# Kernel tuning notes

Measured on AMD Instinct MI355X. Metric: run time of the kernel, lower is better.

## Reference

```python
import jax, jax.numpy as jnp
import numpy as np

NUM_HEADS = 12

def setup_inputs() -> dict:
    key = jax.random.key(0)
    ks = jax.random.split(key, 6)
    B, Nq, Nkv, C = 2, 2048, 2048, 768
    q_token = jax.random.normal(ks[0], (B, Nq, C), dtype=jnp.float32)
    kv_token = jax.random.normal(ks[1], (B, Nkv, C), dtype=jnp.float32)
    s = 1.0 / np.sqrt(C)
    Wq = jax.random.normal(ks[2], (C, C), dtype=jnp.float32) * s
    Wkv = jax.random.normal(ks[3], (C, 2 * C), dtype=jnp.float32) * s
    Wproj = jax.random.normal(ks[4], (C, C), dtype=jnp.float32) * s
    bproj = jnp.zeros((C,), dtype=jnp.float32)
    return {"q_token": q_token, "kv_token": kv_token, "Wq": Wq, "Wkv": Wkv, "Wproj": Wproj, "bproj": bproj}

def reference(q_token, kv_token, Wq, Wkv, Wproj, bproj):
    B, Nq, C = q_token.shape
    H = NUM_HEADS
    D = C // H
    scale = D ** -0.5
    # Q: [B, H, Nq, D]
    Q = (q_token @ Wq).reshape(B, Nq, H, D).transpose(0, 2, 1, 3)
    # KV: token layout is (2, H, D) on last dim -> [2, B, H, Nkv, D]
    Nkv = kv_token.shape[1]
    KV = (kv_token @ Wkv).reshape(B, Nkv, 2, H, D).transpose(2, 0, 3, 1, 4)
    K, V = KV[0], KV[1]
    attn = jnp.einsum('bhqd,bhkd->bhqk', Q, K) * scale
    attn = jax.nn.softmax(attn, axis=-1)
    # NOTE: original code multiplies by scale again here (faithful quirk)
    x = jnp.einsum('bhqk,bhkd->bhqd', attn, V) * scale
    x = x.transpose(0, 2, 1, 3).reshape(B, Nq, C)
    return x @ Wproj + bproj
```

## Files before the change

kernel.cpp:

```cpp
#include <hip/hip_runtime.h>

typedef __attribute__((ext_vector_type(8))) short short8;
typedef __attribute__((ext_vector_type(4))) float f32x4;
typedef __attribute__((ext_vector_type(16))) float f32x16;
typedef __attribute__((ext_vector_type(4))) unsigned u32x4;

__device__ __forceinline__ unsigned short f2bf(float f) {
  unsigned u = __builtin_bit_cast(unsigned, f);
  u += 0x7fffu + ((u >> 16) & 1u);
  return (unsigned short)(u >> 16);
}

__device__ __forceinline__ unsigned cvt_pk_bf16(float a, float b) {
  unsigned r;
  asm("v_cvt_pk_bf16_f32 %0, %1, %2" : "=v"(r) : "v"(a), "v"(b));
  return r;
}

__device__ __forceinline__ void gload_lds16(const unsigned short* g, unsigned short* l) {
  __builtin_amdgcn_global_load_lds((const __attribute__((address_space(1))) unsigned int*)g,
                                   (__attribute__((address_space(3))) unsigned int*)l, 16, 0, 0);
}

__global__ __launch_bounds__(256) void cvt_tr(
    const float* __restrict__ q_token, const float* __restrict__ kv_token,
    const float* __restrict__ Wq, const float* __restrict__ Wkv, const float* __restrict__ Wp,
    unsigned short* __restrict__ qb, unsigned short* __restrict__ kvb,
    unsigned short* __restrict__ wqT, unsigned short* __restrict__ wkvT,
    unsigned short* __restrict__ wpT) {
  __shared__ float tile[32][33];
  const int tid = threadIdx.x;
  int bx = blockIdx.x;
  if (bx < 6144) {
    int i = bx * 256 + tid;
    const float* in = (i < 786432) ? q_token : kv_token;
    unsigned short* out = (i < 786432) ? qb : kvb;
    int j = (i < 786432) ? i : i - 786432;
    float4 v = ((const float4*)in)[j];
    ushort4 o;
    o.x = f2bf(v.x); o.y = f2bf(v.y); o.z = f2bf(v.z); o.w = f2bf(v.w);
    ((ushort4*)out)[j] = o;
    return;
  }
  bx -= 6144;
  int gx = bx % 96, gy = bx / 96;
  const float* in; unsigned short* out; int C;
  if (gx < 24)       { in = Wq;  out = wqT;  C = 768;  }
  else if (gx < 72)  { in = Wkv; out = wkvT; C = 1536; gx -= 24; }
  else               { in = Wp;  out = wpT;  C = 768;  gx -= 72; }
  const int R = 768;
  int c0 = gx * 32, r0 = gy * 32;
  int tx = tid & 31, ty = tid >> 5;
  for (int i = ty; i < 32; i += 8)
    tile[i][tx] = in[(size_t)(r0 + i) * C + c0 + tx];
  __syncthreads();
  for (int i = ty; i < 32; i += 8)
    out[(size_t)(c0 + i) * R + r0 + tx] = f2bf(tile[tx][i]);
}

__global__ __launch_bounds__(256) void gemm_qkv(
    const unsigned short* __restrict__ Aq, const unsigned short* __restrict__ Akv,
    const unsigned short* __restrict__ BtQ, const unsigned short* __restrict__ BtKV,
    unsigned short* __restrict__ Qo, unsigned short* __restrict__ Ko,
    unsigned short* __restrict__ Vo) {
  __shared__ __align__(16) unsigned short A_lds[128][64];
  __shared__ __align__(16) unsigned short B_lds[64][64];
  const bool isQ = blockIdx.y < 12;
  const unsigned short* A  = isQ ? Aq : Akv;
  const unsigned short* Bt = isQ ? BtQ : BtKV;
  const int yy = isQ ? blockIdx.y : blockIdx.y - 12;
  const int K = 768;
  const int tile_m = blockIdx.x * 128;
  const int tile_n = yy * 64;
  const int tid = threadIdx.x;
  const int wid = tid >> 6, lane = tid & 63;
  const int wm = (wid >> 1) * 64, wn = (wid & 1) * 32;
  const int lr = lane & 15, lg = lane >> 4;
  const int s_row = (lane >> 3);
  const int s_col = (lane & 7) * 8;
  f32x4 acc[4][2] = {};

  for (int k0 = 0; k0 < K; k0 += 64) {
    __syncthreads();
#pragma unroll
    for (int j = 0; j < 6; ++j) {
      const int c = wid * 6 + j;
      if (c < 16) {
        const int row = c * 8 + s_row;
        gload_lds16(&A[(size_t)(tile_m + row) * K + k0 + s_col], &A_lds[0][0] + c * 512);
      } else {
        const int row = (c - 16) * 8 + s_row;
        gload_lds16(&Bt[(size_t)(tile_n + row) * K + k0 + s_col], &B_lds[0][0] + (c - 16) * 512);
      }
    }
    __syncthreads();
    short8 a[4][2], b[2][2];
#pragma unroll
    for (int i = 0; i < 4; ++i)
#pragma unroll
      for (int t = 0; t < 2; ++t)
        a[i][t] = *(const short8*)&A_lds[wm + i * 16 + lr][t * 32 + lg * 8];
#pragma unroll
    for (int j = 0; j < 2; ++j)
#pragma unroll
      for (int t = 0; t < 2; ++t)
        b[j][t] = *(const short8*)&B_lds[wn + j * 16 + lr][t * 32 + lg * 8];
#pragma unroll
    for (int i = 0; i < 4; ++i)
#pragma unroll
      for (int j = 0; j < 2; ++j)
#pragma unroll
        for (int t = 0; t < 2; ++t)
          acc[i][j] = __builtin_amdgcn_mfma_f32_16x16x32_bf16(a[i][t], b[j][t], acc[i][j], 0, 0, 0);
  }

#pragma unroll
  for (int i = 0; i < 4; ++i)
#pragma unroll
    for (int j = 0; j < 2; ++j)
#pragma unroll
      for (int r = 0; r < 4; ++r) {
        int m = tile_m + wm + i * 16 + lg * 4 + r;
        int n = tile_n + wn + j * 16 + lr;
        float v = acc[i][j][r];
        int b = m >> 11, row = m & 2047;
        if (isQ) {
          int h = n >> 6, d = n & 63;
          Qo[((size_t)((b * 12 + h) * 2048 + row) << 6) + d] = f2bf(v);
        } else {
          if (n < 768) {
            int h = n >> 6, d = n & 63;
            Ko[((size_t)((b * 12 + h) * 2048 + row) << 6) + d] = f2bf(v);
          } else {
            int h = (n - 768) >> 6, d = n & 63;
            int rowp = (row & ~12) | ((row & 4) << 1) | ((row & 8) >> 1);
            Vo[((size_t)((b * 12 + h) * 64 + d) << 11) + rowp] = f2bf(v);
          }
        }
      }
}

__global__ __launch_bounds__(256) void gemm_proj(
    const unsigned short* __restrict__ A, const unsigned short* __restrict__ Bt,
    float* __restrict__ outf, const float* __restrict__ bias) {
  __shared__ __align__(16) unsigned short A_lds[64][64];
  __shared__ __align__(16) unsigned short B_lds[64][64];
  const int K = 768, N = 768;
  const int tile_m = blockIdx.x * 64;
  const int tile_n = blockIdx.y * 64;
  const int tid = threadIdx.x;
  const int wid = tid >> 6, lane = tid & 63;
  const int wm = (wid >> 1) * 32, wn = (wid & 1) * 32;
  const int lr = lane & 15, lg = lane >> 4;
  const int s_r8 = lane >> 3;
  const int s_col = (lane & 7) * 8;
  f32x4 acc[2][2] = {};

  for (int k0 = 0; k0 < K; k0 += 64) {
    __syncthreads();
#pragma unroll
    for (int i = 0; i < 2; ++i) {
      const int row = (wid * 2 + i) * 8 + s_r8;
      gload_lds16(&A[(size_t)(tile_m + row) * K + k0 + s_col], &A_lds[0][0] + (wid * 2 + i) * 512);
      gload_lds16(&Bt[(size_t)(tile_n + row) * K + k0 + s_col], &B_lds[0][0] + (wid * 2 + i) * 512);
    }
    __syncthreads();
    short8 a[2][2], b[2][2];
#pragma unroll
    for (int i = 0; i < 2; ++i)
#pragma unroll
      for (int t = 0; t < 2; ++t) {
        a[i][t] = *(const short8*)&A_lds[wm + i * 16 + lr][t * 32 + lg * 8];
        b[i][t] = *(const short8*)&B_lds[wn + i * 16 + lr][t * 32 + lg * 8];
      }
#pragma unroll
    for (int i = 0; i < 2; ++i)
#pragma unroll
      for (int j = 0; j < 2; ++j)
#pragma unroll
        for (int t = 0; t < 2; ++t)
          acc[i][j] = __builtin_amdgcn_mfma_f32_16x16x32_bf16(a[i][t], b[j][t], acc[i][j], 0, 0, 0);
  }

#pragma unroll
  for (int i = 0; i < 2; ++i)
#pragma unroll
    for (int j = 0; j < 2; ++j)
#pragma unroll
      for (int r = 0; r < 4; ++r) {
        int m = tile_m + wm + i * 16 + lg * 4 + r;
        int n = tile_n + wn + j * 16 + lr;
        outf[(size_t)m * N + n] = acc[i][j][r] + bias[n];
      }
}

__global__ __launch_bounds__(256, 3) void attn_fwd(
    const unsigned short* __restrict__ Q, const unsigned short* __restrict__ Kb,
    const unsigned short* __restrict__ Vt, unsigned short* __restrict__ X) {
  __shared__ __align__(16) unsigned short SMEM[16384];
  __shared__ float m_lds[4][32];
  __shared__ float l_lds[4][64];
  const int bid = blockIdx.x;
  const int bh = bid % 24;
  const int q0 = (bid / 24) * 64;
  const int tid = threadIdx.x, wid = tid >> 6, lane = tid & 63;
  const int l31 = lane & 31, hi = lane >> 5;
  const int grp = wid >> 1;
  const int qsub = wid & 1;
  const float Cc = 0.18033688011112042f;
  const float THRS = 44.3614195558365f;

  const unsigned short* Kbase = Kb + (size_t)bh * (2048 * 64);
  const unsigned short* Vbase = Vt + (size_t)bh * (64 * 2048);

  short8 qf[4];
  {
    const unsigned short* Qp = Q + ((size_t)bh * 2048 + q0 + qsub * 32 + l31) * 64 + hi * 8;
#pragma unroll
    for (int t = 0; t < 4; ++t) qf[t] = *(const short8*)&Qp[t * 16];
  }

  f32x16 accO0 = {}, accO1 = {};
  float m_run = -1e30f, l_run = 0.f;

  const int gtid = tid & 127;
  const int s_row = gtid >> 3;
  const int s_chk = gtid & 7;
  unsigned short* Kst0 = SMEM + grp * 8192;
  unsigned short* Kst1 = SMEM + grp * 8192 + 4096;
  const int fr = l31 & 7;

  {
    const int kvb = grp * 1024;
#pragma unroll
    for (int p = 0; p < 4; ++p) {
      const int row = p * 16 + s_row;
      float4 v = *(const float4*)&Kbase[(size_t)(kvb + row) * 64 + s_chk * 8];
      *(float4*)&Kst0[row * 64 + ((s_chk ^ (row & 7)) << 3)] = v;
    }
  }
  __syncthreads();

  for (int t = 0; t < 16; ++t) {
    const int cur = t & 1;
    const int kv0 = grp * 1024 + t * 64;
    float4 nK[4];
    if (t < 15) {
#pragma unroll
      for (int p = 0; p < 4; ++p) {
        const int row = p * 16 + s_row;
        nK[p] = *(const float4*)&Kbase[(size_t)(kv0 + 64 + row) * 64 + s_chk * 8];
      }
    }
    short8 vf[8];
#pragma unroll
    for (int s = 0; s < 4; ++s) {
      vf[s]     = *(const short8*)&Vbase[(size_t)l31 * 2048 + kv0 + s * 16 + hi * 8];
      vf[4 + s] = *(const short8*)&Vbase[(size_t)(32 + l31) * 2048 + kv0 + s * 16 + hi * 8];
    }
    const unsigned short* KL = cur ? Kst1 : Kst0;
    f32x16 S0 = {}, S1 = {};
    __builtin_amdgcn_s_setprio(1);
#pragma unroll
    for (int t4 = 0; t4 < 4; ++t4) {
      const int ca = ((2 * t4 + hi) ^ fr) << 3;
      short8 k0 = *(const short8*)&KL[l31 * 64 + ca];
      short8 k1 = *(const short8*)&KL[(32 + l31) * 64 + ca];
      S0 = __builtin_amdgcn_mfma_f32_32x32x16_bf16(k0, qf[t4], S0, 0, 0, 0);
      S1 = __builtin_amdgcn_mfma_f32_32x32x16_bf16(k1, qf[t4], S1, 0, 0, 0);
    }
    __builtin_amdgcn_s_setprio(0);
    float mx[8];
#pragma unroll
    for (int g = 0; g < 4; ++g) {
      mx[g]     = fmaxf(fmaxf(S0[4 * g], S0[4 * g + 1]), fmaxf(S0[4 * g + 2], S0[4 * g + 3]));
      mx[4 + g] = fmaxf(fmaxf(S1[4 * g], S1[4 * g + 1]), fmaxf(S1[4 * g + 2], S1[4 * g + 3]));
    }
    float rmax = fmaxf(fmaxf(fmaxf(mx[0], mx[1]), fmaxf(mx[2], mx[3])),
                       fmaxf(fmaxf(mx[4], mx[5]), fmaxf(mx[6], mx[7])));
    rmax = fmaxf(rmax, __shfl_xor(rmax, 32));
    if (!__all(rmax <= m_run + THRS)) {
      float mnew = fmaxf(m_run, rmax);
      float alpha = exp2f((m_run - mnew) * Cc);
      m_run = mnew;
      l_run *= alpha;
#pragma unroll
      for (int r = 0; r < 16; ++r) { accO0[r] *= alpha; accO1[r] *= alpha; }
    }
    const float mC = m_run * Cc;
#pragma unroll
    for (int r = 0; r < 16; ++r) {
      S0[r] = exp2f(fmaf(S0[r], Cc, -mC));
      S1[r] = exp2f(fmaf(S1[r], Cc, -mC));
    }
    float ts[8];
#pragma unroll
    for (int g = 0; g < 4; ++g) {
      ts[g]     = (S0[4 * g] + S0[4 * g + 1]) + (S0[4 * g + 2] + S0[4 * g + 3]);
      ts[4 + g] = (S1[4 * g] + S1[4 * g + 1]) + (S1[4 * g + 2] + S1[4 * g + 3]);
    }
    l_run += ((ts[0] + ts[1]) + (ts[2] + ts[3])) + ((ts[4] + ts[5]) + (ts[6] + ts[7]));
    unsigned w0[8], w1[8];
#pragma unroll
    for (int j = 0; j < 4; ++j) {
      w0[j]     = cvt_pk_bf16(S0[4 * j],     S0[4 * j + 1]);
      w1[j]     = cvt_pk_bf16(S0[4 * j + 2], S0[4 * j + 3]);
      w0[4 + j] = cvt_pk_bf16(S1[4 * j],     S1[4 * j + 1]);
      w1[4 + j] = cvt_pk_bf16(S1[4 * j + 2], S1[4 * j + 3]);
    }
    __builtin_amdgcn_s_setprio(1);
#pragma unroll
    for (int s = 0; s < 4; ++s) {
      u32x4 pw = {w0[2 * s], w1[2 * s], w0[2 * s + 1], w1[2 * s + 1]};
      short8 pfrag = __builtin_bit_cast(short8, pw);
      accO0 = __builtin_amdgcn_mfma_f32_32x32x16_bf16(vf[s], pfrag, accO0, 0, 0, 0);
      accO1 = __builtin_amdgcn_mfma_f32_32x32x16_bf16(vf[4 + s], pfrag, accO1, 0, 0, 0);
    }
    __builtin_amdgcn_s_setprio(0);
    if (t < 15) {
      unsigned short* KN = cur ? Kst0 : Kst1;
#pragma unroll
      for (int p = 0; p < 4; ++p) {
        const int row = p * 16 + s_row;
        *(float4*)&KN[row * 64 + ((s_chk ^ (row & 7)) << 3)] = nK[p];
      }
    }
    __syncthreads();
  }

  float* Ob = (float*)SMEM;
#pragma unroll
  for (int dt = 0; dt < 2; ++dt) {
    const f32x16& acc = dt ? accO1 : accO0;
#pragma unroll
    for (int r = 0; r < 16; ++r)
      Ob[wid * 2048 + (dt * 16 + r) * 64 + hi * 32 + l31] = acc[r];
  }
  if (hi == 0) m_lds[wid][l31] = m_run;
  l_lds[wid][hi * 32 + l31] = l_run;
  __syncthreads();

  {
    const int qs = wid >> 1, dh = wid & 1;
    const int sl0 = qs, sl1 = qs + 2;
    float m0 = m_lds[sl0][l31], m1 = m_lds[sl1][l31];
    float M = fmaxf(m0, m1);
    float w0s = exp2f((m0 - M) * Cc);
    float w1s = exp2f((m1 - M) * Cc);
    float ltot = w0s * (l_lds[sl0][l31] + l_lds[sl0][32 + l31])
               + w1s * (l_lds[sl1][l31] + l_lds[sl1][32 + l31]);
    const float inv = 0.125f / ltot;
    const int b = bh / 12, h = bh % 12;
    short8 os0, os1;
#pragma unroll
    for (int j = 0; j < 16; ++j) {
      const int d = dh * 32 + hi * 16 + j;
      const int dt = d >> 5, crow = d & 31;
      const int hs = (crow >> 2) & 1;
      const int rr = (crow & 3) | ((crow >> 3) << 2);
      float v = w0s * Ob[sl0 * 2048 + (dt * 16 + rr) * 64 + hs * 32 + l31]
              + w1s * Ob[sl1 * 2048 + (dt * 16 + rr) * 64 + hs * 32 + l31];
      if (j < 8) os0[j] = (short)f2bf(v * inv);
      else       os1[j - 8] = (short)f2bf(v * inv);
    }
    const int q = q0 + qs * 32 + l31;
    unsigned short* Xp = X + ((size_t)b * 2048 + q) * 768 + h * 64 + dh * 32 + hi * 16;
    *(short8*)Xp = os0;
    *(short8*)(Xp + 8) = os1;
  }
}

extern "C" void kernel_launch(void* const* d_in, const int* in_sizes, int n_in,
                              void* d_out, int out_size, void* d_ws, size_t ws_size,
                              hipStream_t stream) {
  const float* q_token  = (const float*)d_in[0];
  const float* kv_token = (const float*)d_in[1];
  const float* Wq    = (const float*)d_in[2];
  const float* Wkv   = (const float*)d_in[3];
  const float* Wproj = (const float*)d_in[4];
  const float* bproj = (const float*)d_in[5];
  float* out = (float*)d_out;

  unsigned short* qb   = (unsigned short*)d_ws;
  unsigned short* kvb  = qb   + 3145728;
  unsigned short* wqT  = kvb  + 3145728;
  unsigned short* wkvT = wqT  + 589824;
  unsigned short* wpT  = wkvT + 1179648;
  unsigned short* Qb   = wpT  + 589824;
  unsigned short* Kbf  = Qb   + 3145728;
  unsigned short* Vtb  = Kbf  + 3145728;
  unsigned short* Xb   = Vtb  + 3145728;

  cvt_tr<<<8448, 256, 0, stream>>>(q_token, kv_token, Wq, Wkv, Wproj,
                                   qb, kvb, wqT, wkvT, wpT);

  gemm_qkv<<<dim3(32, 36), 256, 0, stream>>>(qb, kvb, wqT, wkvT, Qb, Kbf, Vtb);

  attn_fwd<<<768, 256, 0, stream>>>(Qb, Kbf, Vtb, Xb);

  gemm_proj<<<dim3(64, 12), 256, 0, stream>>>(Xb, wpT, out, bproj);
}
```

Measured before the change: 121.2 us.

## Double-buffer LDS tiles in QKV and projection GEMMs to overlap loads with MFMA

```diff
diff --git a/kernel.cpp b/kernel.cpp
--- a/kernel.cpp
+++ b/kernel.cpp
@@ -63,8 +63,8 @@
     const unsigned short* __restrict__ BtQ, const unsigned short* __restrict__ BtKV,
     unsigned short* __restrict__ Qo, unsigned short* __restrict__ Ko,
     unsigned short* __restrict__ Vo) {
-  __shared__ __align__(16) unsigned short A_lds[128][64];
-  __shared__ __align__(16) unsigned short B_lds[64][64];
+  __shared__ __align__(16) unsigned short A_lds[2][8192];
+  __shared__ __align__(16) unsigned short B_lds[2][4096];
   const bool isQ = blockIdx.y < 12;
   const unsigned short* A  = isQ ? Aq : Akv;
   const unsigned short* Bt = isQ ? BtQ : BtKV;
@@ -80,31 +80,36 @@
   const int s_col = (lane & 7) * 8;
   f32x4 acc[4][2] = {};
 
-  for (int k0 = 0; k0 < K; k0 += 64) {
-    __syncthreads();
-#pragma unroll
-    for (int j = 0; j < 6; ++j) {
-      const int c = wid * 6 + j;
-      if (c < 16) {
-        const int row = c * 8 + s_row;
-        gload_lds16(&A[(size_t)(tile_m + row) * K + k0 + s_col], &A_lds[0][0] + c * 512);
-      } else {
-        const int row = (c - 16) * 8 + s_row;
-        gload_lds16(&Bt[(size_t)(tile_n + row) * K + k0 + s_col], &B_lds[0][0] + (c - 16) * 512);
-      }
-    }
-    __syncthreads();
+#define QKV_STAGE(BUF, KOFF)                                                            \
+  _Pragma("unroll")                                                                     \
+  for (int j = 0; j < 6; ++j) {                                                         \
+    const int c = wid * 6 + j;                                                          \
+    if (c < 16) {                                                                       \
+      const int row = c * 8 + s_row;                                                    \
+      gload_lds16(&A[(size_t)(tile_m + row) * K + (KOFF) + s_col], &A_lds[BUF][0] + c * 512); \
+    } else {                                                                            \
+      const int row = (c - 16) * 8 + s_row;                                             \
+      gload_lds16(&Bt[(size_t)(tile_n + row) * K + (KOFF) + s_col], &B_lds[BUF][0] + (c - 16) * 512); \
+    }                                                                                   \
+  }
+
+  QKV_STAGE(0, 0)
+  __syncthreads();
+
+  for (int ks = 0; ks < 12; ++ks) {
+    const int cur = ks & 1;
+    if (ks < 11) { QKV_STAGE(cur ^ 1, (ks + 1) * 64) }
     short8 a[4][2], b[2][2];
 #pragma unroll
     for (int i = 0; i < 4; ++i)
 #pragma unroll
       for (int t = 0; t < 2; ++t)
-        a[i][t] = *(const short8*)&A_lds[wm + i * 16 + lr][t * 32 + lg * 8];
+        a[i][t] = *(const short8*)&A_lds[cur][(wm + i * 16 + lr) * 64 + t * 32 + lg * 8];
 #pragma unroll
     for (int j = 0; j < 2; ++j)
 #pragma unroll
       for (int t = 0; t < 2; ++t)
-        b[j][t] = *(const short8*)&B_lds[wn + j * 16 + lr][t * 32 + lg * 8];
+        b[j][t] = *(const short8*)&B_lds[cur][(wn + j * 16 + lr) * 64 + t * 32 + lg * 8];
 #pragma unroll
     for (int i = 0; i < 4; ++i)
 #pragma unroll
@@ -112,7 +117,9 @@
 #pragma unroll
         for (int t = 0; t < 2; ++t)
           acc[i][j] = __builtin_amdgcn_mfma_f32_16x16x32_bf16(a[i][t], b[j][t], acc[i][j], 0, 0, 0);
-  }
+    __syncthreads();
+  }
+#undef QKV_STAGE
 
 #pragma unroll
   for (int i = 0; i < 4; ++i)
@@ -143,8 +150,8 @@
 __global__ __launch_bounds__(256) void gemm_proj(
     const unsigned short* __restrict__ A, const unsigned short* __restrict__ Bt,
     float* __restrict__ outf, const float* __restrict__ bias) {
-  __shared__ __align__(16) unsigned short A_lds[64][64];
-  __shared__ __align__(16) unsigned short B_lds[64][64];
+  __shared__ __align__(16) unsigned short A_lds[2][4096];
+  __shared__ __align__(16) unsigned short B_lds[2][4096];
   const int K = 768, N = 768;
   const int tile_m = blockIdx.x * 64;
   const int tile_n = blockIdx.y * 64;
@@ -156,22 +163,27 @@
   const int s_col = (lane & 7) * 8;
   f32x4 acc[2][2] = {};
 
-  for (int k0 = 0; k0 < K; k0 += 64) {
-    __syncthreads();
-#pragma unroll
-    for (int i = 0; i < 2; ++i) {
-      const int row = (wid * 2 + i) * 8 + s_r8;
-      gload_lds16(&A[(size_t)(tile_m + row) * K + k0 + s_col], &A_lds[0][0] + (wid * 2 + i) * 512);
-      gload_lds16(&Bt[(size_t)(tile_n + row) * K + k0 + s_col], &B_lds[0][0] + (wid * 2 + i) * 512);
-    }
-    __syncthreads();
+#define PROJ_STAGE(BUF, KOFF)                                                           \
+  _Pragma("unroll")                                                                     \
+  for (int i = 0; i < 2; ++i) {                                                         \
+    const int row = (wid * 2 + i) * 8 + s_r8;                                           \
+    gload_lds16(&A[(size_t)(tile_m + row) * K + (KOFF) + s_col], &A_lds[BUF][0] + (wid * 2 + i) * 512); \
+    gload_lds16(&Bt[(size_t)(tile_n + row) * K + (KOFF) + s_col], &B_lds[BUF][0] + (wid * 2 + i) * 512); \
+  }
+
+  PROJ_STAGE(0, 0)
+  __syncthreads();
+
+  for (int ks = 0; ks < 12; ++ks) {
+    const int cur = ks & 1;
+    if (ks < 11) { PROJ_STAGE(cur ^ 1, (ks + 1) * 64) }
     short8 a[2][2], b[2][2];
 #pragma unroll
     for (int i = 0; i < 2; ++i)
 #pragma unroll
       for (int t = 0; t < 2; ++t) {
-        a[i][t] = *(const short8*)&A_lds[wm + i * 16 + lr][t * 32 + lg * 8];
-        b[i][t] = *(const short8*)&B_lds[wn + i * 16 + lr][t * 32 + lg * 8];
+        a[i][t] = *(const short8*)&A_lds[cur][(wm + i * 16 + lr) * 64 + t * 32 + lg * 8];
+        b[i][t] = *(const short8*)&B_lds[cur][(wn + i * 16 + lr) * 64 + t * 32 + lg * 8];
       }
 #pragma unroll
     for (int i = 0; i < 2; ++i)
@@ -180,7 +192,9 @@
 #pragma unroll
         for (int t = 0; t < 2; ++t)
           acc[i][j] = __builtin_amdgcn_mfma_f32_16x16x32_bf16(a[i][t], b[j][t], acc[i][j], 0, 0, 0);
-  }
+    __syncthreads();
+  }
+#undef PROJ_STAGE
 
 #pragma unroll
   for (int i = 0; i < 2; ++i)
```

Result: slower. 127.7 us (+5.4%).
